# Kernel tuning notes

Hardware: AMD Instinct MI355X
Metric: run time of the kernel (lower is better)

## Reference

```python
import jax, jax.numpy as jnp
import numpy as np

B, T, H = 4096, 2048, 64  # batch, max seq len, hidden size
IN = 1                    # decoder input hardcoded to width 1 in source
BOT = 3                   # latent bottleneck (linear_enc: H->3, linear_dec: 3->H)


def setup_inputs() -> dict:
    key = jax.random.key(0)
    ks = jax.random.split(key, 16)
    s = 1.0 / np.sqrt(H)
    u = lambda k, shape: jax.random.uniform(k, shape, jnp.float32, -s, s)
    padded = jax.random.normal(ks[0], (B, T, IN), jnp.float32)
    seq_lengths = jax.random.randint(ks[1], (B,), 1, T + 1).at[0].set(T)  # max == T (static unroll)
    return {
        "padded": padded,
        "seq_lengths": seq_lengths,
        # encoder LSTM (gate order i,f,g,o like torch); biases b_ih+b_hh fused
        "enc_Wih": u(ks[2], (4 * H, IN)),
        "enc_Whh": u(ks[3], (4 * H, H)),
        "enc_b":   u(ks[4], (4 * H,)),
        # encoder bottleneck linear H->3
        "enc_linW": u(ks[5], (BOT, H)),
        "enc_linb": u(ks[6], (BOT,)),
        # decoder expand linear 3->H
        "dec_linW": u(ks[7], (H, BOT)),
        "dec_linb": u(ks[8], (H,)),
        # decoder LSTM
        "dec_Wih": u(ks[9], (4 * H, IN)),
        "dec_Whh": u(ks[10], (4 * H, H)),
        "dec_b":   u(ks[11], (4 * H,)),
        # output linear H->1
        "outW": u(ks[12], (IN, H)),
        "outb": u(ks[13], (IN,)),
    }


def _lstm_cell(x, h, c, Wih, Whh, b):
    g = x @ Wih.T + h @ Whh.T + b
    i, f, gg, o = jnp.split(g, 4, axis=-1)
    c = jax.nn.sigmoid(f) * c + jax.nn.sigmoid(i) * jnp.tanh(gg)
    h = jax.nn.sigmoid(o) * jnp.tanh(c)
    return h, c


def reference(padded, seq_lengths, enc_Wih, enc_Whh, enc_b, enc_linW, enc_linb,
              dec_linW, dec_linb, dec_Wih, dec_Whh, dec_b, outW, outb):
    Bn, Tn, _ = padded.shape
    Hn = enc_Whh.shape[1]
    xs = jnp.transpose(padded, (1, 0, 2))                       # (T, B, 1)
    mask = jnp.arange(Tn)[:, None] < seq_lengths[None, :]        # (T, B)

    # ---- encoder: packed semantics == freeze (h,c) past each seq's length ----
    h0 = jnp.zeros((Bn, Hn), padded.dtype)
    def enc_step(carry, xm):
        h, c = carry
        x, m = xm
        nh, nc = _lstm_cell(x, h, c, enc_Wih, enc_Whh, enc_b)
        m = m[:, None]
        return (jnp.where(m, nh, h), jnp.where(m, nc, c)), None
    (h, c), _ = jax.lax.scan(enc_step, (h0, h0), (xs, mask))

    hz = jax.nn.sigmoid(h @ enc_linW.T + enc_linb)               # (B, 3) latent

    hd = hz @ dec_linW.T + dec_linb                              # (B, H)
    x0 = jnp.zeros((Bn, 1), padded.dtype)
    def dec_step(carry, _):
        x, hh, cc = carry
        nh, nc = _lstm_cell(x, hh, cc, dec_Wih, dec_Whh, dec_b)
        y = nh @ outW.T + outb
        return (y, nh, nc), y
    _, ys = jax.lax.scan(dec_step, (x0, hd, c), None, length=Tn)  # (T, B, 1)
    output = jnp.transpose(ys, (1, 0, 2))                         # (B, T, 1)

    # ---- masked MSE ----
    maskf = mask.T[:, :, None].astype(padded.dtype)               # (B, T, 1)
    loss = (((padded - output) ** 2) * maskf).sum() / maskf.sum()
    return loss, padded, output, hz[None]
```

## Files before the change

kernel.cpp:

```cpp
#include <hip/hip_runtime.h>

#define B 4096
#define T 2048
#define H 64
#define NBATCH 16
#define NB (B / NBATCH)
#define NTHREADS 1024

typedef __attribute__((ext_vector_type(8))) short short8;
typedef __attribute__((ext_vector_type(4))) float f32x4;

__device__ __forceinline__ float ex2(float x) { return __builtin_amdgcn_exp2f(x); }
__device__ __forceinline__ float sigm(float x) {
    return __builtin_amdgcn_rcpf(1.0f + ex2(-1.4426950408889634f * x));
}
__device__ __forceinline__ float tanh_(float x) {
    float xc = fminf(15.0f, fmaxf(-15.0f, x));
    float e = ex2(2.8853900817779268f * xc);
    return (e - 1.0f) * __builtin_amdgcn_rcpf(e + 1.0f);
}
__device__ __forceinline__ unsigned short f2bf(float f) {
    unsigned u = __builtin_bit_cast(unsigned, f);
    u += 0x7fffu + ((u >> 16) & 1u);
    return (unsigned short)(u >> 16);
}
__device__ __forceinline__ void lds_barrier() {
    asm volatile("s_waitcnt lgkmcnt(0)\n\ts_barrier" ::: "memory");
}

extern "C" __global__ void __launch_bounds__(NTHREADS, 1)
enc_kernel(const float* __restrict__ padded, const int* __restrict__ seq_len,
           const float* __restrict__ Wih, const float* __restrict__ Whh,
           const float* __restrict__ bias,
           float* __restrict__ h_out, float* __restrict__ c_out)
{
    __shared__ unsigned short hA[2][NBATCH][72];
    __shared__ int slen[NBATCH];

    const int tid = threadIdx.x;
    const int w = tid >> 6, L = tid & 63, lo = L & 15, hi = L >> 4;
    const int b0 = blockIdx.x * NBATCH;
    const int unit = w * 4 + hi;

    short8 af[2];
    {
        const int G = (lo & 3) * 64 + w * 4 + (lo >> 2);
        #pragma unroll
        for (int kk = 0; kk < 2; ++kk) {
            const float* src = Whh + (long)G * H + kk * 32 + hi * 8;
            short8 f;
            #pragma unroll
            for (int j = 0; j < 8; ++j) f[j] = (short)f2bf(src[j]);
            af[kk] = f;
        }
    }
    float b_g[4], wi_g[4];
    #pragma unroll
    for (int r = 0; r < 4; ++r) {
        const int G2 = r * 64 + unit;
        b_g[r] = bias[G2];
        wi_g[r] = Wih[G2];
    }

    if (tid < NBATCH * 64) hA[0][tid >> 6][tid & 63] = 0;
    if (tid < NBATCH) slen[tid] = seq_len[b0 + tid];
    lds_barrier();

    int maxlen = 1;
    #pragma unroll
    for (int i = 0; i < NBATCH; ++i) maxlen = max(maxlen, slen[i]);
    const int len_lo = slen[lo];

    const float* xrow = padded + (long)(b0 + lo) * T;
    f32x4 xc = *(const f32x4*)(xrow);
    f32x4 xn = *(const f32x4*)(xrow + 4);

    float c_st = 0.f, h_st = 0.f;

#define ESTEP(P, XI)                                                          \
    {                                                                         \
        const float x = xc[XI];                                               \
        short8 hb0 = *(const short8*)&hA[P][lo][hi * 8];                      \
        short8 hb1 = *(const short8*)&hA[P][lo][32 + hi * 8];                 \
        f32x4 z = {b_g[0] + wi_g[0] * x, b_g[1] + wi_g[1] * x,                \
                   b_g[2] + wi_g[2] * x, b_g[3] + wi_g[3] * x};               \
        z = __builtin_amdgcn_mfma_f32_16x16x32_bf16(af[0], hb0, z, 0,0,0);    \
        f32x4 acc = __builtin_amdgcn_mfma_f32_16x16x32_bf16(af[1], hb1, z, 0,0,0); \
        const bool act = (t + XI) < len_lo;                                   \
        float i_ = sigm(acc[0]);                                              \
        float f_ = sigm(acc[1]);                                              \
        float g_ = tanh_(acc[2]);                                             \
        float o_ = sigm(acc[3]);                                              \
        float cn = f_ * c_st + i_ * g_;                                       \
        float hn = o_ * tanh_(cn);                                            \
        if (act) { c_st = cn; h_st = hn; }                                    \
        hA[(P) ^ 1][lo][unit] = f2bf(h_st);                                   \
        lds_barrier();                                                        \
    }

    for (int t = 0; t < maxlen; t += 4) {
        int nb = t + 8; if (nb > T - 4) nb = T - 4;
        f32x4 xf = *(const f32x4*)(xrow + nb);
        ESTEP(0, 0) ESTEP(1, 1) ESTEP(0, 2) ESTEP(1, 3)
        xc = xn; xn = xf;
    }
#undef ESTEP

    h_out[(long)(b0 + lo) * H + unit] = h_st;
    c_out[(long)(b0 + lo) * H + unit] = c_st;
}

extern "C" __global__ void __launch_bounds__(256)
mid_kernel(const float* __restrict__ h_enc,
           const float* __restrict__ eW, const float* __restrict__ eb,
           const float* __restrict__ dW, const float* __restrict__ db,
           const float* __restrict__ outW, const float* __restrict__ outb,
           float* __restrict__ hz_out, float* __restrict__ hd_out,
           float* __restrict__ y0c)
{
    int b = blockIdx.x * blockDim.x + threadIdx.x;
    if (b >= B) return;
    const float* h = h_enc + (long)b * H;
    float hz[3];
    #pragma unroll
    for (int j = 0; j < 3; ++j) {
        float s = eb[j];
        for (int k = 0; k < H; ++k) s += h[k] * eW[j*H + k];
        hz[j] = sigm(s);
        hz_out[b*3 + j] = hz[j];
    }
    float y0 = outb[0];
    for (int u = 0; u < H; ++u) {
        float hd = db[u] + hz[0]*dW[u*3] + hz[1]*dW[u*3+1] + hz[2]*dW[u*3+2];
        hd_out[(long)b*H + u] = hd;
        y0 += outW[u] * hd;
    }
    y0c[b] = y0;
}

extern "C" __global__ void __launch_bounds__(NTHREADS, 1)
dec_kernel(const float* __restrict__ hd, const float* __restrict__ c_in,
           const float* __restrict__ Wih, const float* __restrict__ Whh,
           const float* __restrict__ bias, const float* __restrict__ outW,
           const float* __restrict__ outb, const float* __restrict__ y0c,
           float* __restrict__ y_out)
{
    __shared__ unsigned short hA[2][NBATCH][72];

    const int tid = threadIdx.x;
    const int w = tid >> 6, L = tid & 63, lo = L & 15, hi = L >> 4;
    const int b0 = blockIdx.x * NBATCH;
    const int unit = w * 4 + hi;

    short8 af[2];
    {
        const int G = (lo & 3) * 64 + w * 4 + (lo >> 2);
        const float wir = Wih[G];
        #pragma unroll
        for (int kk = 0; kk < 2; ++kk) {
            const float* src = Whh + (long)G * H + kk * 32 + hi * 8;
            const float* ow  = outW + kk * 32 + hi * 8;
            short8 f;
            #pragma unroll
            for (int j = 0; j < 8; ++j) f[j] = (short)f2bf(src[j] + wir * ow[j]);
            af[kk] = f;
        }
    }
    const float outb_s = outb[0];
    const float y0 = y0c[b0 + lo];
    float b_g[4], corr[4];
    #pragma unroll
    for (int r = 0; r < 4; ++r) {
        const int G2 = r * 64 + unit;
        const float wir = Wih[G2];
        b_g[r] = bias[G2] + wir * outb_s;
        corr[r] = wir * y0;
    }
    short8 ya[2];
    #pragma unroll
    for (int kk = 0; kk < 2; ++kk) {
        short8 f = (short8)0;
        if (lo == 0)
            #pragma unroll
            for (int j = 0; j < 8; ++j) f[j] = (short)f2bf(outW[kk*32 + hi*8 + j]);
        ya[kk] = f;
    }

    if (tid < NBATCH * 64) {
        int m = tid >> 6, k = tid & 63;
        hA[0][m][k] = f2bf(hd[(long)(b0 + m) * H + k]);
    }
    float c_st = c_in[(long)(b0 + lo) * H + unit];
    lds_barrier();

#define DSTEP(P, CORR, TT)                                                    \
    {                                                                         \
        short8 hb0 = *(const short8*)&hA[P][lo][hi * 8];                      \
        short8 hb1 = *(const short8*)&hA[P][lo][32 + hi * 8];                 \
        f32x4 z = {b_g[0], b_g[1], b_g[2], b_g[3]};                           \
        z = __builtin_amdgcn_mfma_f32_16x16x32_bf16(af[0], hb0, z, 0,0,0);    \
        f32x4 acc = __builtin_amdgcn_mfma_f32_16x16x32_bf16(af[1], hb1, z, 0,0,0); \
        if (w == ((TT) & 15)) {     \
            f32x4 zy = {outb_s, outb_s, outb_s, outb_s};                      \
            zy = __builtin_amdgcn_mfma_f32_16x16x32_bf16(ya[0], hb0, zy, 0,0,0); \
            zy = __builtin_amdgcn_mfma_f32_16x16x32_bf16(ya[1], hb1, zy, 0,0,0); \
            if ((TT) > 0 && hi == 0)                                          \
                y_out[(long)(b0 + lo) * T + ((TT) - 1)] = zy[0];              \
        }                                                                     \
        if (CORR) {                                                           \
            _Pragma("unroll")                                                 \
            for (int r = 0; r < 4; ++r) acc[r] -= corr[r];                    \
        }                                                                     \
        float i_ = sigm(acc[0]);                                              \
        float f_ = sigm(acc[1]);                                              \
        float g_ = tanh_(acc[2]);                                             \
        float o_ = sigm(acc[3]);                                              \
        float cn = f_ * c_st + i_ * g_;                                       \
        float hn = o_ * tanh_(cn);                                            \
        c_st = cn;                                                            \
        hA[(P) ^ 1][lo][unit] = f2bf(hn);                                     \
        lds_barrier();                                                        \
    }

    DSTEP(0, 1, 0) DSTEP(1, 0, 1) DSTEP(0, 0, 2) DSTEP(1, 0, 3)
    for (int t = 4; t < T; t += 4) {
        DSTEP(0, 0, t) DSTEP(1, 0, t + 1) DSTEP(0, 0, t + 2) DSTEP(1, 0, t + 3)
    }
#undef DSTEP

    if (w == 0) {
        short8 hb0 = *(const short8*)&hA[0][lo][hi * 8];
        short8 hb1 = *(const short8*)&hA[0][lo][32 + hi * 8];
        f32x4 zy = {outb_s, outb_s, outb_s, outb_s};
        zy = __builtin_amdgcn_mfma_f32_16x16x32_bf16(ya[0], hb0, zy, 0,0,0);
        zy = __builtin_amdgcn_mfma_f32_16x16x32_bf16(ya[1], hb1, zy, 0,0,0);
        if (hi == 0) y_out[(long)(b0 + lo) * T + (T - 1)] = zy[0];
    }
}

extern "C" __global__ void __launch_bounds__(256)
loss_kernel(const float* __restrict__ padded, const float* __restrict__ y,
            const int* __restrict__ seq_len, float* __restrict__ acc2)
{
    const long n4 = (long)B * T / 4;
    long i0 = (long)(blockIdx.x * blockDim.x + threadIdx.x);
    long stride = (long)gridDim.x * blockDim.x;
    float s = 0.f, cnt = 0.f;
    for (long i = i0; i < n4; i += stride) {
        int b = (int)(i >> 9);
        int t = (int)(i & 511) * 4;
        int len = seq_len[b];
        f32x4 pv = *(const f32x4*)&padded[i * 4];
        f32x4 yv = *(const f32x4*)&y[i * 4];
        #pragma unroll
        for (int e = 0; e < 4; ++e)
            if (t + e < len) { float d = pv[e] - yv[e]; s += d * d; cnt += 1.0f; }
    }
    for (int m = 1; m < 64; m <<= 1) { s += __shfl_xor(s, m); cnt += __shfl_xor(cnt, m); }
    if ((threadIdx.x & 63) == 0) { atomicAdd(&acc2[0], s); atomicAdd(&acc2[1], cnt); }
}

extern "C" __global__ void fin_kernel(const float* __restrict__ acc2, float* __restrict__ out)
{
    out[0] = acc2[0] / acc2[1];
}

extern "C" void kernel_launch(void* const* d_in, const int* in_sizes, int n_in,
                              void* d_out, int out_size, void* d_ws, size_t ws_size,
                              hipStream_t stream)
{
    const float* padded = (const float*)d_in[0];
    const int*   seq    = (const int*)  d_in[1];
    const float* eWih   = (const float*)d_in[2];
    const float* eWhh   = (const float*)d_in[3];
    const float* eb     = (const float*)d_in[4];
    const float* elW    = (const float*)d_in[5];
    const float* elb    = (const float*)d_in[6];
    const float* dlW    = (const float*)d_in[7];
    const float* dlb    = (const float*)d_in[8];
    const float* dWih   = (const float*)d_in[9];
    const float* dWhh   = (const float*)d_in[10];
    const float* db     = (const float*)d_in[11];
    const float* outW   = (const float*)d_in[12];
    const float* outb   = (const float*)d_in[13];
    float* out = (float*)d_out;

    float* ws    = (float*)d_ws;
    float* h_enc = ws;
    float* c_enc = ws + (long)B * H;
    float* hd    = ws + 2L * B * H;
    float* y0c   = ws + 3L * B * H;
    float* acc2  = ws + 3L * B * H + B;

    float* out_pad = out + 1;
    float* out_y   = out + 1 + (long)B * T;
    float* out_hz  = out + 1 + 2L * (long)B * T;

    hipMemcpyAsync(out_pad, padded, (long)B * T * sizeof(float),
                   hipMemcpyDeviceToDevice, stream);
    hipMemsetAsync(acc2, 0, 2 * sizeof(float), stream);

    enc_kernel<<<NB, NTHREADS, 0, stream>>>(padded, seq, eWih, eWhh, eb, h_enc, c_enc);
    mid_kernel<<<B / 256, 256, 0, stream>>>(h_enc, elW, elb, dlW, dlb, outW, outb,
                                            out_hz, hd, y0c);
    dec_kernel<<<NB, NTHREADS, 0, stream>>>(hd, c_enc, dWih, dWhh, db, outW, outb, y0c, out_y);
    loss_kernel<<<1024, 256, 0, stream>>>(padded, out_y, seq, acc2);
    fin_kernel<<<1, 1, 0, stream>>>(acc2, out);
}
```

Measured before the change: 2.003 ms.

## Halve batch per block, duplicate batch columns across MFMA halves, cheaper tanh

Each block now handles 8 sequences with 512 threads instead of 16 with 1024. The 16-wide MFMA N dimension holds the 8 batches twice, so each wave computes two 4-unit row tiles and each lane selects the half it owns. With 512 blocks and a launch bound allowing up to 4 blocks per CU, more CUs get work and several independent recurrences can interleave around the per-step barriers. This costs redundant MFMA work, since half of every result is discarded, and extra registers. tanh is also rewritten as 2*sigmoid(2x)-1 without clamping, removing a few instructions on the critical path.

```diff
diff --git a/kernel.cpp b/kernel.cpp
--- a/kernel.cpp
+++ b/kernel.cpp
@@ -3,9 +3,9 @@
 #define B 4096
 #define T 2048
 #define H 64
-#define NBATCH 16
+#define NBATCH 8
 #define NB (B / NBATCH)
-#define NTHREADS 1024
+#define NTHREADS 512
 
 typedef __attribute__((ext_vector_type(8))) short short8;
 typedef __attribute__((ext_vector_type(4))) float f32x4;
@@ -15,9 +15,8 @@
     return __builtin_amdgcn_rcpf(1.0f + ex2(-1.4426950408889634f * x));
 }
 __device__ __forceinline__ float tanh_(float x) {
-    float xc = fminf(15.0f, fmaxf(-15.0f, x));
-    float e = ex2(2.8853900817779268f * xc);
-    return (e - 1.0f) * __builtin_amdgcn_rcpf(e + 1.0f);
+    return __builtin_fmaf(2.0f,
+        __builtin_amdgcn_rcpf(1.0f + ex2(-2.8853900817779268f * x)), -1.0f);
 }
 __device__ __forceinline__ unsigned short f2bf(float f) {
     unsigned u = __builtin_bit_cast(unsigned, f);
@@ -28,7 +27,7 @@
     asm volatile("s_waitcnt lgkmcnt(0)\n\ts_barrier" ::: "memory");
 }
 
-extern "C" __global__ void __launch_bounds__(NTHREADS, 1)
+extern "C" __global__ void __launch_bounds__(NTHREADS, 4)
 enc_kernel(const float* __restrict__ padded, const int* __restrict__ seq_len,
            const float* __restrict__ Wih, const float* __restrict__ Whh,
            const float* __restrict__ bias,
@@ -40,38 +39,43 @@
     const int tid = threadIdx.x;
     const int w = tid >> 6, L = tid & 63, lo = L & 15, hi = L >> 4;
     const int b0 = blockIdx.x * NBATCH;
-    const int unit = w * 4 + hi;
-
-    short8 af[2];
-    {
-        const int G = (lo & 3) * 64 + w * 4 + (lo >> 2);
+    const int bat = lo & 7;
+    const bool hiT = lo >= 8;
+    const int unit = w * 8 + (hiT ? 4 : 0) + hi;
+
+    short8 af[2][2];
+    #pragma unroll
+    for (int rt = 0; rt < 2; ++rt) {
+        const int G = (lo & 3) * 64 + w * 8 + rt * 4 + (lo >> 2);
         #pragma unroll
         for (int kk = 0; kk < 2; ++kk) {
             const float* src = Whh + (long)G * H + kk * 32 + hi * 8;
             short8 f;
             #pragma unroll
             for (int j = 0; j < 8; ++j) f[j] = (short)f2bf(src[j]);
-            af[kk] = f;
+            af[rt][kk] = f;
         }
     }
-    float b_g[4], wi_g[4];
-    #pragma unroll
-    for (int r = 0; r < 4; ++r) {
-        const int G2 = r * 64 + unit;
-        b_g[r] = bias[G2];
-        wi_g[r] = Wih[G2];
-    }
-
-    if (tid < NBATCH * 64) hA[0][tid >> 6][tid & 63] = 0;
+    float b_g[2][4], wi_g[2][4];
+    #pragma unroll
+    for (int rt = 0; rt < 2; ++rt)
+        #pragma unroll
+        for (int r = 0; r < 4; ++r) {
+            const int G2 = r * 64 + w * 8 + rt * 4 + hi;
+            b_g[rt][r] = bias[G2];
+            wi_g[rt][r] = Wih[G2];
+        }
+
+    hA[0][tid >> 6][tid & 63] = 0;
     if (tid < NBATCH) slen[tid] = seq_len[b0 + tid];
     lds_barrier();
 
     int maxlen = 1;
     #pragma unroll
     for (int i = 0; i < NBATCH; ++i) maxlen = max(maxlen, slen[i]);
-    const int len_lo = slen[lo];
-
-    const float* xrow = padded + (long)(b0 + lo) * T;
+    const int len_lo = slen[bat];
+
+    const float* xrow = padded + (long)(b0 + bat) * T;
     f32x4 xc = *(const f32x4*)(xrow);
     f32x4 xn = *(const f32x4*)(xrow + 4);
 
@@ -80,21 +84,29 @@
 #define ESTEP(P, XI)                                                          \
     {                                                                         \
         const float x = xc[XI];                                               \
-        short8 hb0 = *(const short8*)&hA[P][lo][hi * 8];                      \
-        short8 hb1 = *(const short8*)&hA[P][lo][32 + hi * 8];                 \
-        f32x4 z = {b_g[0] + wi_g[0] * x, b_g[1] + wi_g[1] * x,                \
-                   b_g[2] + wi_g[2] * x, b_g[3] + wi_g[3] * x};               \
-        z = __builtin_amdgcn_mfma_f32_16x16x32_bf16(af[0], hb0, z, 0,0,0);    \
-        f32x4 acc = __builtin_amdgcn_mfma_f32_16x16x32_bf16(af[1], hb1, z, 0,0,0); \
+        short8 hb0 = *(const short8*)&hA[P][bat][hi * 8];                     \
+        short8 hb1 = *(const short8*)&hA[P][bat][32 + hi * 8];                \
+        f32x4 z0 = {b_g[0][0] + wi_g[0][0] * x, b_g[0][1] + wi_g[0][1] * x,   \
+                    b_g[0][2] + wi_g[0][2] * x, b_g[0][3] + wi_g[0][3] * x};  \
+        f32x4 z1 = {b_g[1][0] + wi_g[1][0] * x, b_g[1][1] + wi_g[1][1] * x,   \
+                    b_g[1][2] + wi_g[1][2] * x, b_g[1][3] + wi_g[1][3] * x};  \
+        z0 = __builtin_amdgcn_mfma_f32_16x16x32_bf16(af[0][0], hb0, z0, 0,0,0); \
+        z1 = __builtin_amdgcn_mfma_f32_16x16x32_bf16(af[1][0], hb0, z1, 0,0,0); \
+        z0 = __builtin_amdgcn_mfma_f32_16x16x32_bf16(af[0][1], hb1, z0, 0,0,0); \
+        z1 = __builtin_amdgcn_mfma_f32_16x16x32_bf16(af[1][1], hb1, z1, 0,0,0); \
         const bool act = (t + XI) < len_lo;                                   \
-        float i_ = sigm(acc[0]);                                              \
-        float f_ = sigm(acc[1]);                                              \
-        float g_ = tanh_(acc[2]);                                             \
-        float o_ = sigm(acc[3]);                                              \
+        const float a0 = hiT ? z1[0] : z0[0];                                 \
+        const float a1 = hiT ? z1[1] : z0[1];                                 \
+        const float a2 = hiT ? z1[2] : z0[2];                                 \
+        const float a3 = hiT ? z1[3] : z0[3];                                 \
+        float i_ = sigm(a0);                                                  \
+        float f_ = sigm(a1);                                                  \
+        float g_ = tanh_(a2);                                                 \
+        float o_ = sigm(a3);                                                  \
         float cn = f_ * c_st + i_ * g_;                                       \
         float hn = o_ * tanh_(cn);                                            \
         if (act) { c_st = cn; h_st = hn; }                                    \
-        hA[(P) ^ 1][lo][unit] = f2bf(h_st);                                   \
+        hA[(P) ^ 1][bat][unit] = f2bf(h_st);                                  \
         lds_barrier();                                                        \
     }
 
@@ -106,8 +118,8 @@
     }
 #undef ESTEP
 
-    h_out[(long)(b0 + lo) * H + unit] = h_st;
-    c_out[(long)(b0 + lo) * H + unit] = c_st;
+    h_out[(long)(b0 + bat) * H + unit] = h_st;
+    c_out[(long)(b0 + bat) * H + unit] = c_st;
 }
 
 extern "C" __global__ void __launch_bounds__(256)
@@ -138,7 +150,7 @@
     y0c[b] = y0;
 }
 
-extern "C" __global__ void __launch_bounds__(NTHREADS, 1)
+extern "C" __global__ void __launch_bounds__(NTHREADS, 4)
 dec_kernel(const float* __restrict__ hd, const float* __restrict__ c_in,
            const float* __restrict__ Wih, const float* __restrict__ Whh,
            const float* __restrict__ bias, const float* __restrict__ outW,
@@ -150,11 +162,14 @@
     const int tid = threadIdx.x;
     const int w = tid >> 6, L = tid & 63, lo = L & 15, hi = L >> 4;
     const int b0 = blockIdx.x * NBATCH;
-    const int unit = w * 4 + hi;
-
-    short8 af[2];
-    {
-        const int G = (lo & 3) * 64 + w * 4 + (lo >> 2);
+    const int bat = lo & 7;
+    const bool hiT = lo >= 8;
+    const int unit = w * 8 + (hiT ? 4 : 0) + hi;
+
+    short8 af[2][2];
+    #pragma unroll
+    for (int rt = 0; rt < 2; ++rt) {
+        const int G = (lo & 3) * 64 + w * 8 + rt * 4 + (lo >> 2);
         const float wir = Wih[G];
         #pragma unroll
         for (int kk = 0; kk < 2; ++kk) {
@@ -163,19 +178,24 @@
             short8 f;
             #pragma unroll
             for (int j = 0; j < 8; ++j) f[j] = (short)f2bf(src[j] + wir * ow[j]);
-            af[kk] = f;
+            af[rt][kk] = f;
         }
     }
     const float outb_s = outb[0];
-    const float y0 = y0c[b0 + lo];
-    float b_g[4], corr[4];
-    #pragma unroll
-    for (int r = 0; r < 4; ++r) {
-        const int G2 = r * 64 + unit;
-        const float wir = Wih[G2];
-        b_g[r] = bias[G2] + wir * outb_s;
-        corr[r] = wir * y0;
-    }
+    const float y0 = y0c[b0 + bat];
+    float zb[2][4];
+    #pragma unroll
+    for (int rt = 0; rt < 2; ++rt)
+        #pragma unroll
+        for (int r = 0; r < 4; ++r) {
+            const int G2 = r * 64 + w * 8 + rt * 4 + hi;
+            zb[rt][r] = bias[G2] + Wih[G2] * outb_s;
+        }
+    float corr[4];
+    #pragma unroll
+    for (int r = 0; r < 4; ++r)
+        corr[r] = Wih[r * 64 + unit] * y0;
+
     short8 ya[2];
     #pragma unroll
     for (int kk = 0; kk < 2; ++kk) {
@@ -186,39 +206,40 @@
         ya[kk] = f;
     }
 
-    if (tid < NBATCH * 64) {
-        int m = tid >> 6, k = tid & 63;
-        hA[0][m][k] = f2bf(hd[(long)(b0 + m) * H + k]);
-    }
-    float c_st = c_in[(long)(b0 + lo) * H + unit];
+    hA[0][tid >> 6][tid & 63] = f2bf(hd[(long)(b0 + (tid >> 6)) * H + (tid & 63)]);
+    float c_st = c_in[(long)(b0 + bat) * H + unit];
     lds_barrier();
 
 #define DSTEP(P, CORR, TT)                                                    \
     {                                                                         \
-        short8 hb0 = *(const short8*)&hA[P][lo][hi * 8];                      \
-        short8 hb1 = *(const short8*)&hA[P][lo][32 + hi * 8];                 \
-        f32x4 z = {b_g[0], b_g[1], b_g[2], b_g[3]};                           \
-        z = __builtin_amdgcn_mfma_f32_16x16x32_bf16(af[0], hb0, z, 0,0,0);    \
-        f32x4 acc = __builtin_amdgcn_mfma_f32_16x16x32_bf16(af[1], hb1, z, 0,0,0); \
-        if (w == ((TT) & 15)) {     \
+        short8 hb0 = *(const short8*)&hA[P][bat][hi * 8];                     \
+        short8 hb1 = *(const short8*)&hA[P][bat][32 + hi * 8];                \
+        f32x4 z0 = {zb[0][0], zb[0][1], zb[0][2], zb[0][3]};                  \
+        f32x4 z1 = {zb[1][0], zb[1][1], zb[1][2], zb[1][3]};                  \
+        z0 = __builtin_amdgcn_mfma_f32_16x16x32_bf16(af[0][0], hb0, z0, 0,0,0); \
+        z1 = __builtin_amdgcn_mfma_f32_16x16x32_bf16(af[1][0], hb0, z1, 0,0,0); \
+        z0 = __builtin_amdgcn_mfma_f32_16x16x32_bf16(af[0][1], hb1, z0, 0,0,0); \
+        z1 = __builtin_amdgcn_mfma_f32_16x16x32_bf16(af[1][1], hb1, z1, 0,0,0); \
+        if (w == ((TT) & 7)) {      \
             f32x4 zy = {outb_s, outb_s, outb_s, outb_s};                      \
             zy = __builtin_amdgcn_mfma_f32_16x16x32_bf16(ya[0], hb0, zy, 0,0,0); \
             zy = __builtin_amdgcn_mfma_f32_16x16x32_bf16(ya[1], hb1, zy, 0,0,0); \
-            if ((TT) > 0 && hi == 0)                                          \
+            if ((TT) > 0 && hi == 0 && lo < 8)                                \
                 y_out[(long)(b0 + lo) * T + ((TT) - 1)] = zy[0];              \
         }                                                                     \
-        if (CORR) {                                                           \
-            _Pragma("unroll")                                                 \
-            for (int r = 0; r < 4; ++r) acc[r] -= corr[r];                    \
-        }                                                                     \
-        float i_ = sigm(acc[0]);                                              \
-        float f_ = sigm(acc[1]);                                              \
-        float g_ = tanh_(acc[2]);                                             \
-        float o_ = sigm(acc[3]);                                              \
+        float a0 = hiT ? z1[0] : z0[0];                                       \
+        float a1 = hiT ? z1[1] : z0[1];                                       \
+        float a2 = hiT ? z1[2] : z0[2];                                       \
+        float a3 = hiT ? z1[3] : z0[3];                                       \
+        if (CORR) { a0 -= corr[0]; a1 -= corr[1]; a2 -= corr[2]; a3 -= corr[3]; } \
+        float i_ = sigm(a0);                                                  \
+        float f_ = sigm(a1);                                                  \
+        float g_ = tanh_(a2);                                                 \
+        float o_ = sigm(a3);                                                  \
         float cn = f_ * c_st + i_ * g_;                                       \
         float hn = o_ * tanh_(cn);                                            \
         c_st = cn;                                                            \
-        hA[(P) ^ 1][lo][unit] = f2bf(hn);                                     \
+        hA[(P) ^ 1][bat][unit] = f2bf(hn);                                    \
         lds_barrier();                                                        \
     }
 
@@ -229,12 +250,12 @@
 #undef DSTEP
 
     if (w == 0) {
-        short8 hb0 = *(const short8*)&hA[0][lo][hi * 8];
-        short8 hb1 = *(const short8*)&hA[0][lo][32 + hi * 8];
+        short8 hb0 = *(const short8*)&hA[0][bat][hi * 8];
+        short8 hb1 = *(const short8*)&hA[0][bat][32 + hi * 8];
         f32x4 zy = {outb_s, outb_s, outb_s, outb_s};
         zy = __builtin_amdgcn_mfma_f32_16x16x32_bf16(ya[0], hb0, zy, 0,0,0);
         zy = __builtin_amdgcn_mfma_f32_16x16x32_bf16(ya[1], hb1, zy, 0,0,0);
-        if (hi == 0) y_out[(long)(b0 + lo) * T + (T - 1)] = zy[0];
+        if (hi == 0 && lo < 8) y_out[(long)(b0 + lo) * T + (T - 1)] = zy[0];
     }
 }
 
```

Measured after the change: 2.077 ms. 3.7% more time.
